# Kernel tuning notes

Measured on AMD Instinct MI355X. Metric: run time of the kernel, lower is better.

## Reference

```python
import jax, jax.numpy as jnp
import numpy as np

N = 50000   # nodes
E = 800000  # edges (avg degree 16)
D = 64      # in_feat
OUT = 64    # out_feat


def _layernorm(x, gamma, beta, eps=1e-5):
    m = jnp.mean(x, axis=-1, keepdims=True)
    v = jnp.mean((x - m) ** 2, axis=-1, keepdims=True)  # biased var, as torch LayerNorm
    return (x - m) * jax.lax.rsqrt(v + eps) * gamma + beta


def setup_inputs() -> dict:
    key = jax.random.key(0)
    ks = jax.random.split(key, 6)
    s1 = 1.0 / np.sqrt(D)
    s2 = 1.0 / np.sqrt(2 * D)
    return {
        "x": jax.random.normal(ks[0], (N, D), dtype=jnp.float32),
        "edge_index": jax.random.randint(ks[1], (2, E), 0, N, dtype=jnp.int64),
        "W1a": jax.random.normal(ks[2], (D, D), dtype=jnp.float32) * s1,
        "W1b": jax.random.normal(ks[3], (D, D), dtype=jnp.float32) * s1,
        "gamma1": jnp.ones((D,), jnp.float32),
        "beta1": jnp.zeros((D,), jnp.float32),
        "w": jnp.ones((D,), jnp.float32),
        "gamma2": jnp.ones((D,), jnp.float32),
        "beta2": jnp.zeros((D,), jnp.float32),
        "W2a": jax.random.normal(ks[4], (D, 2 * D), dtype=jnp.float32) * s2,
        "W2b": jax.random.normal(ks[5], (OUT, D), dtype=jnp.float32) * s1,
    }


def reference(x, edge_index, W1a, W1b, gamma1, beta1, w, gamma2, beta2, W2a, W2b):
    row, col = edge_index[0], edge_index[1]
    n = x.shape[0]
    # gather -> MLP1 (two bias-free linears with ReLU)
    msg = x[row]                                        # [E, D]
    msg = jax.nn.relu(msg @ W1a.T) @ W1b.T              # [E, D]
    # scatter_mean over destination nodes
    s = jax.ops.segment_sum(msg, col, num_segments=n)   # [N, D]
    cnt = jax.ops.segment_sum(jnp.ones((col.shape[0],), x.dtype), col, num_segments=n)
    agg = s / jnp.maximum(cnt, 1.0)[:, None]
    agg = _layernorm(agg, gamma1, beta1)
    # repulsion + residual + LayerNorm
    fx = _layernorm(x + (x - agg) * w, gamma2, beta2)
    # concat -> MLP2
    h = jnp.concatenate([fx, agg], axis=1)              # [N, 2D]
    return jax.nn.relu(h @ W2a.T) @ W2b.T               # [N, OUT]
```

## Files before the change

### kernel.cpp

```cpp
#include <hip/hip_runtime.h>
#include <hip/hip_bf16.h>

#define NN 50000
#define NE 800000
#define CAP 48
#define BINS 3125
#define HROW 3126
#define P1B 391
#define CHUNK 2048
#define MLPB 768
#define SUPT 782
#define HIDX(b) ((b) + ((b) >> 4))

typedef short v8s __attribute__((ext_vector_type(8)));
typedef float v4f __attribute__((ext_vector_type(4)));
#define MFMA16(a, b, c) __builtin_amdgcn_mfma_f32_16x16x32_bf16(a, b, c, 0, 0, 0)

__device__ __forceinline__ float bfu2f(unsigned short u) {
    union { unsigned int i; float f; } v; v.i = ((unsigned int)u) << 16; return v.f;
}
__device__ __forceinline__ unsigned short f2bf_rne(float f) {
    union { float f; unsigned int i; } v; v.f = f;
    unsigned int x = v.i;
    unsigned int r = x + 0x7fffu + ((x >> 16) & 1u);
    return (unsigned short)(r >> 16);
}
__device__ __forceinline__ v8s fragf32(const float* p) {
    float4 u = ((const float4*)p)[0];
    float4 v = ((const float4*)p)[1];
    v8s r;
    r[0] = (short)f2bf_rne(u.x); r[1] = (short)f2bf_rne(u.y);
    r[2] = (short)f2bf_rne(u.z); r[3] = (short)f2bf_rne(u.w);
    r[4] = (short)f2bf_rne(v.x); r[5] = (short)f2bf_rne(v.y);
    r[6] = (short)f2bf_rne(v.z); r[7] = (short)f2bf_rne(v.w);
    return r;
}
__device__ __forceinline__ v8s fragbf(const unsigned short* p) {
    union { uint4 u; v8s s; } t; t.u = *((const uint4*)p); return t.s;
}
__device__ __forceinline__ v4f vzero() { v4f z; z[0]=0.f; z[1]=0.f; z[2]=0.f; z[3]=0.f; return z; }

__global__ __launch_bounds__(256) void p1fat_k(const int* __restrict__ ei,
                                               const float* __restrict__ x,
                                               const float* __restrict__ W1a,
                                               const float* __restrict__ W1b,
                                               unsigned int* __restrict__ chunkbuf,
                                               unsigned short* __restrict__ histT,
                                               unsigned short* __restrict__ y) {
    __shared__ __align__(16) unsigned int smem[8448];
    int t = threadIdx.x;
    if (blockIdx.x < P1B) {
        unsigned int*   hcnt  = smem;
        unsigned short* sst16 = (unsigned short*)(smem + 4352);
        unsigned int*   data  = smem + 4352 + 2048;
        unsigned int*   scan  = data;
        int pc = blockIdx.x;
        int e0 = pc * CHUNK;
        int e1 = e0 + CHUNK; if (e1 > NE) e1 = NE;
        int ne = e1 - e0;
        bool i64 = ((ei[1] | ei[3] | ei[5] | ei[7]) == 0);
        for (int i = t; i < 4352; i += 256) hcnt[i] = 0;
        __syncthreads();
        unsigned int packed[8];
#pragma unroll
        for (int i = 0; i < 8; ++i) {
            int e = e0 + t + 256 * i;
            unsigned int pk = 0xFFFFFFFFu;
            if (e < e1) {
                int col = i64 ? ei[2 * (NE + e)] : ei[NE + e];
                int row = i64 ? ei[2 * e]        : ei[e];
                pk = ((unsigned int)col << 16) | (unsigned int)row;
                atomicAdd(&hcnt[HIDX(col >> 4)], 1u);
            }
            packed[i] = pk;
        }
        __syncthreads();
        unsigned int vv[16], tsum = 0;
#pragma unroll
        for (int k = 0; k < 16; ++k) { vv[k] = hcnt[HIDX(16 * t + k)]; tsum += vv[k]; }
        scan[t] = tsum;
        __syncthreads();
        for (int off = 1; off < 256; off <<= 1) {
            unsigned int a = (t >= off) ? scan[t - off] : 0;
            __syncthreads();
            scan[t] += a;
            __syncthreads();
        }
        {
            unsigned int run = scan[t] - tsum;
#pragma unroll
            for (int k = 0; k < 16; ++k) {
                int bb = 16 * t + k;
                hcnt[HIDX(bb)] = run;
                sst16[bb] = (unsigned short)run;
                run += vv[k];
            }
        }
        __syncthreads();
#pragma unroll
        for (int i = 0; i < 8; ++i) {
            unsigned int pk = packed[i];
            if (pk != 0xFFFFFFFFu) {
                unsigned int pos = atomicAdd(&hcnt[HIDX(pk >> 20)], 1u);
                data[pos] = pk;
            }
        }
        __syncthreads();
        unsigned int* cb = chunkbuf + (size_t)pc * CHUNK;
        for (int i = t; i < ne; i += 256) cb[i] = data[i];
        unsigned short* hrow = histT + (size_t)pc * HROW;
        for (int i = t; i < BINS; i += 256) hrow[i] = sst16[i];
        if (t == 0) hrow[BINS] = (unsigned short)ne;
        return;
    }
    unsigned short* wa  = (unsigned short*)smem;
    unsigned short* wb  = wa + 64 * 72;
    unsigned short* h1s = wb + 64 * 72;
    for (int i = t; i < 64 * 64; i += 256) {
        int r = i >> 6, c = i & 63;
        wa[r * 72 + c] = f2bf_rne(W1a[i]);
        wb[r * 72 + c] = f2bf_rne(W1b[i]);
    }
    __syncthreads();
    int w = t >> 6, l = t & 63;
    int lm = l & 15, lq = l >> 4;
    for (int st = blockIdx.x - P1B; st < SUPT; st += MLPB) {
        int nb = st * 64;
        int arow = nb + w * 16 + lm;
        int arc = arow < NN ? arow : NN - 1;
        const float* xr = x + (size_t)arc * 64;
        v8s a0 = fragf32(xr + lq * 8);
        v8s a1 = fragf32(xr + 32 + lq * 8);
        v4f acc[4];
#pragma unroll
        for (int jt = 0; jt < 4; ++jt) acc[jt] = vzero();
#pragma unroll
        for (int jt = 0; jt < 4; ++jt) {
            const unsigned short* wr = &wa[(jt * 16 + lm) * 72];
            acc[jt] = MFMA16(a0, fragbf(wr + lq * 8), acc[jt]);
            acc[jt] = MFMA16(a1, fragbf(wr + 32 + lq * 8), acc[jt]);
        }
#pragma unroll
        for (int jt = 0; jt < 4; ++jt)
#pragma unroll
            for (int r = 0; r < 4; ++r)
                h1s[(w * 16 + lq * 4 + r) * 72 + jt * 16 + lm] = f2bf_rne(fmaxf(acc[jt][r], 0.0f));
        __syncthreads();
        v8s c0 = fragbf(&h1s[(w * 16 + lm) * 72 + lq * 8]);
        v8s c1 = fragbf(&h1s[(w * 16 + lm) * 72 + 32 + lq * 8]);
        v4f acc2[4];
#pragma unroll
        for (int jt = 0; jt < 4; ++jt) acc2[jt] = vzero();
#pragma unroll
        for (int jt = 0; jt < 4; ++jt) {
            const unsigned short* wr = &wb[(jt * 16 + lm) * 72];
            acc2[jt] = MFMA16(c0, fragbf(wr + lq * 8), acc2[jt]);
            acc2[jt] = MFMA16(c1, fragbf(wr + 32 + lq * 8), acc2[jt]);
        }
#pragma unroll
        for (int jt = 0; jt < 4; ++jt)
#pragma unroll
            for (int r = 0; r < 4; ++r) {
                int n = nb + w * 16 + lq * 4 + r;
                if (n < NN) y[(size_t)n * 64 + jt * 16 + lm] = f2bf_rne(acc2[jt][r]);
            }
        __syncthreads();
    }
}

__device__ __forceinline__ float wsum64(float v) {
#pragma unroll
    for (int o = 32; o > 0; o >>= 1) v += __shfl_xor(v, o, 64);
    return v;
}
__device__ __forceinline__ void ln_store(float s0, float s1, int tdeg, int n, int p, int j, int f0,
                                         const float* __restrict__ x,
                                         const float* __restrict__ g1, const float* __restrict__ b1,
                                         const float* __restrict__ wrep,
                                         const float* __restrict__ g2, const float* __restrict__ b2,
                                         unsigned short* __restrict__ h) {
    float inv = 1.0f / (float)(tdeg > 1 ? tdeg : 1);
    float a0 = s0 * inv, a1 = s1 * inv;
    float m = wsum64(a0 + a1) * (1.0f / 128.0f);
    float d0 = a0 - m, d1 = a1 - m;
    float var = wsum64(d0 * d0 + d1 * d1) * (1.0f / 128.0f);
    float r = rsqrtf(var + 1e-5f);
    float2 g1v = *(const float2*)(g1 + f0);
    float2 b1v = *(const float2*)(b1 + f0);
    a0 = d0 * r * g1v.x + b1v.x;
    a1 = d1 * r * g1v.y + b1v.y;
    float2 xv = *(const float2*)(x + (size_t)n * 64 + f0);
    float2 wv = *(const float2*)(wrep + f0);
    float t0 = xv.x + (xv.x - a0) * wv.x;
    float t1 = xv.y + (xv.y - a1) * wv.y;
    float m2 = wsum64(t0 + t1) * (1.0f / 128.0f);
    float e0 = t0 - m2, e1 = t1 - m2;
    float var2 = wsum64(e0 * e0 + e1 * e1) * (1.0f / 128.0f);
    float r2 = rsqrtf(var2 + 1e-5f);
    float2 g2v = *(const float2*)(g2 + f0);
    float2 b2v = *(const float2*)(b2 + f0);
    float fx0 = e0 * r2 * g2v.x + b2v.x;
    float fx1 = e1 * r2 * g2v.y + b2v.y;
    unsigned* hw = (unsigned*)(h + (size_t)n * 128);
    if (p == 0) hw[j]      = (unsigned)f2bf_rne(fx0) | ((unsigned)f2bf_rne(fx1) << 16);
    else        hw[32 + j] = (unsigned)f2bf_rne(a0)  | ((unsigned)f2bf_rne(a1)  << 16);
}

__global__ __launch_bounds__(256) void p2gl_k(const unsigned int* __restrict__ chunkbuf,
                                              const unsigned short* __restrict__ histT,
                                              const unsigned short* __restrict__ y,
                                              const float* __restrict__ x,
                                              const float* __restrict__ g1, const float* __restrict__ b1,
                                              const float* __restrict__ wrep,
                                              const float* __restrict__ g2, const float* __restrict__ b2,
                                              unsigned short* __restrict__ h) {
    __shared__ __align__(16) unsigned int s[400];
    unsigned short* dl = (unsigned short*)s;
    unsigned int*   cl = s + 384;
    int t = threadIdx.x;
    int b = blockIdx.x;
    int n0g = b * 16;
    if (t < 16) cl[t] = 0;
    for (int i = t; i < 384; i += 256) s[i] = 0;
    __syncthreads();
    for (int sg = t; sg < P1B; sg += 256) {
        int st = (int)histT[(size_t)sg * HROW + b];
        int en = (int)histT[(size_t)sg * HROW + b + 1];
        const unsigned int* cb = chunkbuf + (size_t)sg * CHUNK;
        for (int i = st; i < en; ++i) {
            unsigned d = cb[i];
            int c = (int)(d >> 16) - n0g;
            unsigned slot = atomicAdd(&cl[c], 1u);
            if (slot < CAP) dl[c * CAP + slot] = (unsigned short)(d & 0xffffu);
        }
    }
    __syncthreads();
    int w = t >> 6, l = t & 63;
    int p = l >> 5, j = l & 31, f0 = 2 * j;
#pragma unroll
    for (int q = 0; q < 2; ++q) {
        int nl0 = q * 8 + w * 2, nl1 = nl0 + 1;
        int dA = (int)cl[nl0], dB = (int)cl[nl1];
        int eA = dA < CAP ? dA : CAP;
        int eB = dB < CAP ? dB : CAP;
        float sA0 = 0.f, sA1 = 0.f, sB0 = 0.f, sB1 = 0.f;
#pragma unroll
        for (int c6 = 0; c6 < 6; ++c6) {
            bool cA = c6 * 8 < eA, cB = c6 * 8 < eB;
            if (cA | cB) {
#pragma unroll
                for (int i = 0; i < 4; ++i) {
                    int e = c6 * 8 + 2 * i + p;
                    int idA = (int)dl[nl0 * CAP + e];
                    int idB = (int)dl[nl1 * CAP + e];
                    unsigned uA = *(const unsigned*)(y + (size_t)idA * 64 + f0);
                    unsigned uB = *(const unsigned*)(y + (size_t)idB * 64 + f0);
                    bool okA = cA && e < eA, okB = cB && e < eB;
                    sA0 += okA ? bfu2f((unsigned short)(uA & 0xffffu)) : 0.0f;
                    sA1 += okA ? bfu2f((unsigned short)(uA >> 16)) : 0.0f;
                    sB0 += okB ? bfu2f((unsigned short)(uB & 0xffffu)) : 0.0f;
                    sB1 += okB ? bfu2f((unsigned short)(uB >> 16)) : 0.0f;
                }
            }
        }
        sA0 += __shfl_xor(sA0, 32, 64);
        sA1 += __shfl_xor(sA1, 32, 64);
        sB0 += __shfl_xor(sB0, 32, 64);
        sB1 += __shfl_xor(sB1, 32, 64);
        ln_store(sA0, sA1, dA, n0g + nl0, p, j, f0, x, g1, b1, wrep, g2, b2, h);
        ln_store(sB0, sB1, dB, n0g + nl1, p, j, f0, x, g1, b1, wrep, g2, b2, h);
    }
}

__global__ __launch_bounds__(256) void mlp2_k(const unsigned short* hin,
                                              const float* __restrict__ W2a,
                                              const float* __restrict__ W2b,
                                              float* out) {
    __shared__ unsigned short sm2[64 * 136 + 64 * 72 + 64 * 72];
    unsigned short* wa2 = sm2;
    unsigned short* wb2 = wa2 + 64 * 136;
    unsigned short* t2s = wb2 + 64 * 72;
    int t = threadIdx.x;
    for (int i = t; i < 64 * 128; i += 256) {
        int r = i >> 7, c = i & 127;
        wa2[r * 136 + c] = f2bf_rne(W2a[i]);
    }
    for (int i = t; i < 64 * 64; i += 256) {
        int r = i >> 6, c = i & 63;
        wb2[r * 72 + c] = f2bf_rne(W2b[i]);
    }
    __syncthreads();
    int w = t >> 6, l = t & 63;
    int lm = l & 15, lq = l >> 4;
    for (int st = blockIdx.x; st < SUPT; st += MLPB) {
        int nb = st * 64;
        int arow = nb + w * 16 + lm;
        int arc = arow < NN ? arow : NN - 1;
        const unsigned short* fr = hin + (size_t)arc * 128;
        v8s a0 = fragbf(fr + lq * 8);
        v8s a1 = fragbf(fr + 32 + lq * 8);
        v8s a2 = fragbf(fr + 64 + lq * 8);
        v8s a3 = fragbf(fr + 96 + lq * 8);
        v4f acc[4];
#pragma unroll
        for (int jt = 0; jt < 4; ++jt) acc[jt] = vzero();
#pragma unroll
        for (int jt = 0; jt < 4; ++jt) {
            const unsigned short* wr = &wa2[(jt * 16 + lm) * 136];
            acc[jt] = MFMA16(a0, fragbf(wr + lq * 8), acc[jt]);
            acc[jt] = MFMA16(a1, fragbf(wr + 32 + lq * 8), acc[jt]);
            acc[jt] = MFMA16(a2, fragbf(wr + 64 + lq * 8), acc[jt]);
            acc[jt] = MFMA16(a3, fragbf(wr + 96 + lq * 8), acc[jt]);
        }
#pragma unroll
        for (int jt = 0; jt < 4; ++jt)
#pragma unroll
            for (int r = 0; r < 4; ++r)
                t2s[(w * 16 + lq * 4 + r) * 72 + jt * 16 + lm] = f2bf_rne(fmaxf(acc[jt][r], 0.0f));
        __syncthreads();
        v8s c0 = fragbf(&t2s[(w * 16 + lm) * 72 + lq * 8]);
        v8s c1 = fragbf(&t2s[(w * 16 + lm) * 72 + 32 + lq * 8]);
        v4f acc2[4];
#pragma unroll
        for (int jt = 0; jt < 4; ++jt) acc2[jt] = vzero();
#pragma unroll
        for (int jt = 0; jt < 4; ++jt) {
            const unsigned short* wr = &wb2[(jt * 16 + lm) * 72];
            acc2[jt] = MFMA16(c0, fragbf(wr + lq * 8), acc2[jt]);
            acc2[jt] = MFMA16(c1, fragbf(wr + 32 + lq * 8), acc2[jt]);
        }
#pragma unroll
        for (int jt = 0; jt < 4; ++jt)
#pragma unroll
            for (int r = 0; r < 4; ++r) {
                int n = nb + w * 16 + lq * 4 + r;
                if (n < NN) out[(size_t)n * 64 + jt * 16 + lm] = acc2[jt][r];
            }
        __syncthreads();
    }
}

extern "C" void kernel_launch(void* const* d_in, const int* in_sizes, int n_in,
                              void* d_out, int out_size, void* d_ws, size_t ws_size,
                              hipStream_t stream) {
    const float* x   = (const float*)d_in[0];
    const int*   ei  = (const int*)d_in[1];
    const float* W1a = (const float*)d_in[2];
    const float* W1b = (const float*)d_in[3];
    const float* g1  = (const float*)d_in[4];
    const float* b1  = (const float*)d_in[5];
    const float* w   = (const float*)d_in[6];
    const float* g2  = (const float*)d_in[7];
    const float* b2  = (const float*)d_in[8];
    const float* W2a = (const float*)d_in[9];
    const float* W2b = (const float*)d_in[10];

    char* ws = (char*)d_ws;
    unsigned short* y        = (unsigned short*)(ws + 0);
    unsigned int*   chunkbuf = (unsigned int*)(ws + 6400000);
    unsigned short* histT    = (unsigned short*)(ws + 9603072);

    p1fat_k<<<P1B + MLPB, 256, 0, stream>>>(ei, x, W1a, W1b, chunkbuf, histT, y);
    p2gl_k<<<BINS, 256, 0, stream>>>(chunkbuf, histT, y, x, g1, b1, w, g2, b2,
                                     (unsigned short*)d_out);
    mlp2_k<<<MLPB, 256, 0, stream>>>((const unsigned short*)d_out, W2a, W2b, (float*)d_out);
    (void)in_sizes; (void)n_in; (void)out_size; (void)ws_size;
}
```

Before: 138.6 us.

## Keep MLP2 weight fragments in registers, split output columns across waves

The MLP2 kernel no longer stages bf16-converted W2a/W2b in shared memory. Each wave now loads its own 16-column slice of both weight matrices into registers once, converting on the fly with fragf32, and loops over the four 16-row blocks of the tile. This removes the per-block weight staging, its barrier and the repeated LDS weight reads. In exchange each wave now reads every input row of the tile from global memory (four times the A-fragment loads, likely served from cache), and the kernel relies on a fragf32 helper existing elsewhere in the file.

```diff
diff --git a/kernel.cpp b/kernel.cpp
--- a/kernel.cpp
+++ b/kernel.cpp
@@ -276,66 +276,52 @@
                                               const float* __restrict__ W2a,
                                               const float* __restrict__ W2b,
                                               float* out) {
-    __shared__ unsigned short sm2[64 * 136 + 64 * 72 + 64 * 72];
-    unsigned short* wa2 = sm2;
-    unsigned short* wb2 = wa2 + 64 * 136;
-    unsigned short* t2s = wb2 + 64 * 72;
+    __shared__ unsigned short t2s[64 * 72];
     int t = threadIdx.x;
-    for (int i = t; i < 64 * 128; i += 256) {
-        int r = i >> 7, c = i & 127;
-        wa2[r * 136 + c] = f2bf_rne(W2a[i]);
-    }
-    for (int i = t; i < 64 * 64; i += 256) {
-        int r = i >> 6, c = i & 63;
-        wb2[r * 72 + c] = f2bf_rne(W2b[i]);
-    }
-    __syncthreads();
     int w = t >> 6, l = t & 63;
     int lm = l & 15, lq = l >> 4;
+    const float* wra = W2a + (size_t)(w * 16 + lm) * 128;
+    v8s qa0 = fragf32(wra + lq * 8);
+    v8s qa1 = fragf32(wra + 32 + lq * 8);
+    v8s qa2 = fragf32(wra + 64 + lq * 8);
+    v8s qa3 = fragf32(wra + 96 + lq * 8);
+    const float* wrb = W2b + (size_t)(w * 16 + lm) * 64;
+    v8s qb0 = fragf32(wrb + lq * 8);
+    v8s qb1 = fragf32(wrb + 32 + lq * 8);
     for (int st = blockIdx.x; st < SUPT; st += MLPB) {
         int nb = st * 64;
-        int arow = nb + w * 16 + lm;
-        int arc = arow < NN ? arow : NN - 1;
-        const unsigned short* fr = hin + (size_t)arc * 128;
-        v8s a0 = fragbf(fr + lq * 8);
-        v8s a1 = fragbf(fr + 32 + lq * 8);
-        v8s a2 = fragbf(fr + 64 + lq * 8);
-        v8s a3 = fragbf(fr + 96 + lq * 8);
-        v4f acc[4];
-#pragma unroll
-        for (int jt = 0; jt < 4; ++jt) acc[jt] = vzero();
-#pragma unroll
-        for (int jt = 0; jt < 4; ++jt) {
-            const unsigned short* wr = &wa2[(jt * 16 + lm) * 136];
-            acc[jt] = MFMA16(a0, fragbf(wr + lq * 8), acc[jt]);
-            acc[jt] = MFMA16(a1, fragbf(wr + 32 + lq * 8), acc[jt]);
-            acc[jt] = MFMA16(a2, fragbf(wr + 64 + lq * 8), acc[jt]);
-            acc[jt] = MFMA16(a3, fragbf(wr + 96 + lq * 8), acc[jt]);
-        }
-#pragma unroll
-        for (int jt = 0; jt < 4; ++jt)
+#pragma unroll
+        for (int ri = 0; ri < 4; ++ri) {
+            int arow = nb + ri * 16 + lm;
+            int arc = arow < NN ? arow : NN - 1;
+            const unsigned short* fr = hin + (size_t)arc * 128;
+            v8s a0 = fragbf(fr + lq * 8);
+            v8s a1 = fragbf(fr + 32 + lq * 8);
+            v8s a2 = fragbf(fr + 64 + lq * 8);
+            v8s a3 = fragbf(fr + 96 + lq * 8);
+            v4f acc = vzero();
+            acc = MFMA16(a0, qa0, acc);
+            acc = MFMA16(a1, qa1, acc);
+            acc = MFMA16(a2, qa2, acc);
+            acc = MFMA16(a3, qa3, acc);
 #pragma unroll
             for (int r = 0; r < 4; ++r)
-                t2s[(w * 16 + lq * 4 + r) * 72 + jt * 16 + lm] = f2bf_rne(fmaxf(acc[jt][r], 0.0f));
-        __syncthreads();
-        v8s c0 = fragbf(&t2s[(w * 16 + lm) * 72 + lq * 8]);
-        v8s c1 = fragbf(&t2s[(w * 16 + lm) * 72 + 32 + lq * 8]);
-        v4f acc2[4];
-#pragma unroll
-        for (int jt = 0; jt < 4; ++jt) acc2[jt] = vzero();
-#pragma unroll
-        for (int jt = 0; jt < 4; ++jt) {
-            const unsigned short* wr = &wb2[(jt * 16 + lm) * 72];
-            acc2[jt] = MFMA16(c0, fragbf(wr + lq * 8), acc2[jt]);
-            acc2[jt] = MFMA16(c1, fragbf(wr + 32 + lq * 8), acc2[jt]);
-        }
-#pragma unroll
-        for (int jt = 0; jt < 4; ++jt)
+                t2s[(ri * 16 + lq * 4 + r) * 72 + w * 16 + lm] = f2bf_rne(fmaxf(acc[r], 0.0f));
+        }
+        __syncthreads();
+#pragma unroll
+        for (int ri = 0; ri < 4; ++ri) {
+            v8s c0 = fragbf(&t2s[(ri * 16 + lm) * 72 + lq * 8]);
+            v8s c1 = fragbf(&t2s[(ri * 16 + lm) * 72 + 32 + lq * 8]);
+            v4f acc2 = vzero();
+            acc2 = MFMA16(c0, qb0, acc2);
+            acc2 = MFMA16(c1, qb1, acc2);
 #pragma unroll
             for (int r = 0; r < 4; ++r) {
-                int n = nb + w * 16 + lq * 4 + r;
-                if (n < NN) out[(size_t)n * 64 + jt * 16 + lm] = acc2[jt][r];
-            }
+                int n = nb + ri * 16 + lq * 4 + r;
+                if (n < NN) out[(size_t)n * 64 + w * 16 + lm] = acc2[r];
+            }
+        }
         __syncthreads();
     }
 }
```

Measured after the change: 144.9 us. 4.5% more time.
